# Optimization experiments

Measured on AMD Instinct MI355X. Metric: run time of the kernel, lower is better.

Reference implementation:

```python
import jax, jax.numpy as jnp
import numpy as np
from jax import lax

INPUT_DIM = 16
H1, H2 = 64, 32
OUT_DIM = 1
B, T = 4096, 168


def _uniform(key, shape, k):
    return jax.random.uniform(key, shape, jnp.float32, -k, k)


def setup_inputs() -> dict:
    key = jax.random.key(0)
    ks = jax.random.split(key, 12)
    k1 = 1.0 / np.sqrt(H1)
    k2 = 1.0 / np.sqrt(H2)
    return {
        "x": jax.random.normal(ks[0], (B, T, INPUT_DIM), jnp.float32),
        # layer 1 (PyTorch gate order: i, f, g, o)
        "W_ih1": _uniform(ks[1], (4 * H1, INPUT_DIM), k1),
        "W_hh1": _uniform(ks[2], (4 * H1, H1), k1),
        "b_ih1": _uniform(ks[3], (4 * H1,), k1),
        "b_hh1": _uniform(ks[4], (4 * H1,), k1),
        # layer 2
        "W_ih2": _uniform(ks[5], (4 * H2, H1), k2),
        "W_hh2": _uniform(ks[6], (4 * H2, H2), k2),
        "b_ih2": _uniform(ks[7], (4 * H2,), k2),
        "b_hh2": _uniform(ks[8], (4 * H2,), k2),
        # final linear
        "W_fc": _uniform(ks[9], (OUT_DIM, H2), k2),
        "b_fc": _uniform(ks[10], (OUT_DIM,), k2),
    }


def _lstm(x, W_ih, W_hh, b_ih, b_hh, hidden):
    # Precompute input-to-gate projections for all timesteps: [B, T, 4H]
    xg = jnp.einsum("btd,gd->btg", x, W_ih) + b_ih + b_hh

    def step(carry, xt):
        h, c = carry
        gates = xt + h @ W_hh.T  # [B, 4H]
        i, f, g, o = jnp.split(gates, 4, axis=-1)
        i = jax.nn.sigmoid(i)
        f = jax.nn.sigmoid(f)
        g = jnp.tanh(g)
        o = jax.nn.sigmoid(o)
        c = f * c + i * g
        h = o * jnp.tanh(c)
        return (h, c), h

    bsz = x.shape[0]
    init = (jnp.zeros((bsz, hidden), x.dtype), jnp.zeros((bsz, hidden), x.dtype))
    (_, _), hs = lax.scan(step, init, jnp.swapaxes(xg, 0, 1))  # hs: [T, B, H]
    return jnp.swapaxes(hs, 0, 1)  # [B, T, H]


def reference(x, W_ih1, W_hh1, b_ih1, b_hh1, W_ih2, W_hh2, b_ih2, b_hh2, W_fc, b_fc):
    # Dropout layers are identity at inference (p=0.2 in train only).
    h1 = _lstm(x, W_ih1, W_hh1, b_ih1, b_hh1, H1)   # [B, T, 64]
    h2 = _lstm(h1, W_ih2, W_hh2, b_ih2, b_hh2, H2)  # [B, T, 32]
    last = h2[:, -1, :]                              # [B, 32]
    return last @ W_fc.T + b_fc                      # [B, OUT_DIM]
```

## Files before the change

### kernel.cpp

```cpp
#include <hip/hip_runtime.h>


typedef __bf16 bf16x8 __attribute__((ext_vector_type(8)));
typedef float  f32x4  __attribute__((ext_vector_type(4)));

constexpr int T_SEQ = 168;
constexpr int NB    = 16;

__device__ __forceinline__ float fsig(float v)  { return __builtin_amdgcn_rcpf(1.f + __expf(-v)); }
__device__ __forceinline__ float ftanhf(float v){ return 2.f * __builtin_amdgcn_rcpf(1.f + __expf(-2.f * v)) - 1.f; }

__device__ __forceinline__ void split_bf16(float x, __bf16& hi, __bf16& lo) {
  hi = (__bf16)x;
  lo = (__bf16)(x - (float)hi);
}

__device__ __forceinline__ void load_frag8(const float* __restrict__ Wrow, int k0,
                                           bf16x8& hi, bf16x8& lo) {
#pragma unroll
  for (int j = 0; j < 8; ++j) {
    float v = Wrow[k0 + j];
    __bf16 h = (__bf16)v;
    hi[j] = h;
    lo[j] = (__bf16)(v - (float)h);
  }
}

#define MFMA(a, b, c) __builtin_amdgcn_mfma_f32_16x16x32_bf16((a), (b), (c), 0, 0, 0)

__global__ __launch_bounds__(512, 1)
void lstm_mfma_kernel(const float* __restrict__ x,
    const float* __restrict__ Wih1, const float* __restrict__ Whh1,
    const float* __restrict__ bih1, const float* __restrict__ bhh1,
    const float* __restrict__ Wih2, const float* __restrict__ Whh2,
    const float* __restrict__ bih2, const float* __restrict__ bhh2,
    const float* __restrict__ Wfc,  const float* __restrict__ bfc,
    float* __restrict__ out)
{
  __shared__ __align__(16) __bf16 sA1[2][4 * 64 * 8];
  __shared__ __align__(16) __bf16 sA2[2][2 * 64 * 8];
  __shared__ __align__(16) __bf16 sW2[8 * 4 * 64 * 8];
  __shared__ __align__(16) __bf16 sWh2[2 * 4 * 2 * 64 * 8];
  __shared__ __align__(16) float  sP[2 * 4 * 64 * 4];
  __shared__ __align__(16) float  sH2f[16 * 32];

  const int tid  = threadIdx.x;
  const int w    = tid >> 6;
  const int lane = tid & 63;
  const int q    = lane >> 4;
  const int col  = lane & 15;
  const int b0   = blockIdx.x * NB;

  const bool isL1  = (w < 4);
  const bool isL2b = (w == 4) || (w == 5);
  const bool isL2a = (w >= 6);
  const int  wl2b  = w - 4;
  const int  wl2a  = w - 6;

  bf16x8 bhh[4][4];
  bf16x8 bih[4];
  float  b1v[4] = {0.f, 0.f, 0.f, 0.f};
  if (isL1) {
#pragma unroll
    for (int g = 0; g < 4; ++g) {
      const int r = g * 64 + w * 16 + col;
      const float* Wr = Whh1 + r * 64;
      bf16x8 h0, l0, h1f, l1f;
      load_frag8(Wr, 0 * 32 + q * 8, h0, l0);
      load_frag8(Wr, 1 * 32 + q * 8, h1f, l1f);
      bhh[g][0] = h0; bhh[g][1] = h1f; bhh[g][2] = l0; bhh[g][3] = l1f;
      bf16x8 xh, xl;
      load_frag8(Wih1 + r * 16, (q & 1) * 8, xh, xl);
      bih[g] = (q < 2) ? xh : xl;
      b1v[g] = bih1[r] + bhh1[r];
    }
  }
  float b2v[4] = {0.f, 0.f, 0.f, 0.f};
  if (isL2b) {
#pragma unroll
    for (int g = 0; g < 4; ++g) {
      const int r = g * 32 + wl2b * 16 + col;
      b2v[g] = bih2[r] + bhh2[r];
    }
  }

  for (int idx = tid; idx < 8 * 4 * 64; idx += 512) {
    const int nt = idx >> 8;
    const int kb = (idx >> 6) & 3;
    const int ln = idx & 63;
    const int qq = ln >> 4, cc = ln & 15;
    const int g  = nt >> 1, wv = nt & 1;
    const int r  = g * 32 + wv * 16 + cc;
    const int k0 = (kb & 1) * 32 + qq * 8;
    bf16x8 hh, ll;
    load_frag8(Wih2 + r * 64, k0, hh, ll);
    *(bf16x8*)&sW2[((nt * 4 + kb) * 64 + ln) * 8] = (kb < 2) ? hh : ll;
  }
  for (int idx = tid; idx < 2 * 4 * 2 * 64; idx += 512) {
    const int ln = idx & 63;
    const int hl = (idx >> 6) & 1;
    const int g  = (idx >> 7) & 3;
    const int wl = idx >> 9;
    const int qq = ln >> 4, cc = ln & 15;
    const int r  = g * 32 + wl * 16 + cc;
    bf16x8 hh, ll;
    load_frag8(Whh2 + r * 32, qq * 8, hh, ll);
    *(bf16x8*)&sWh2[(((wl * 4 + g) * 2 + hl) * 64 + ln) * 8] = hl ? ll : hh;
  }

  {
    bf16x8 z;
#pragma unroll
    for (int j = 0; j < 8; ++j) z[j] = (__bf16)0.f;
    for (int i = tid; i < 2 * 4 * 64; i += 512) *(bf16x8*)&sA1[0][i * 8] = z;
    for (int i = tid; i < 2 * 2 * 64; i += 512) *(bf16x8*)&sA2[0][i * 8] = z;
  }
  __syncthreads();

  const float* xbase = x + ((size_t)(b0 + col) * T_SEQ) * 16 + (q & 1) * 8;
  float4 xcA, xcB, xnA, xnB;
  if (isL1) {
    xcA = *(const float4*)(xbase + 0);
    xcB = *(const float4*)(xbase + 4);
  }

  float c1s[4] = {0.f, 0.f, 0.f, 0.f};
  float c2s[4] = {0.f, 0.f, 0.f, 0.f};
  const int uu   = w * 16 + col;
  const int uu2b = wl2b * 16 + col;

  for (int t = 0; t <= T_SEQ; ++t) {
    const int p = t & 1;

    if (isL1 && t + 1 < T_SEQ) {
      const float* xr = xbase + (size_t)(t + 1) * 16;
      xnA = *(const float4*)(xr + 0);
      xnB = *(const float4*)(xr + 4);
    }

    if (isL2a && t >= 1) {
      const bf16x8 a2l0 = *(const bf16x8*)&sA1[p][(2 * 64 + lane) * 8];
      const bf16x8 a2l1 = *(const bf16x8*)&sA1[p][(3 * 64 + lane) * 8];
      const bf16x8 ah0  = *(const bf16x8*)&sA2[p][(0 * 64 + lane) * 8];
      const bf16x8 ah1  = *(const bf16x8*)&sA2[p][(1 * 64 + lane) * 8];
#pragma unroll
      for (int g = 0; g < 4; ++g) {
        const int nt = g * 2 + wl2a;
        const bf16x8 whi0 = *(const bf16x8*)&sW2[((nt * 4 + 0) * 64 + lane) * 8];
        const bf16x8 whi1 = *(const bf16x8*)&sW2[((nt * 4 + 1) * 64 + lane) * 8];
        const bf16x8 whh  = *(const bf16x8*)&sWh2[(((wl2a * 4 + g) * 2 + 0) * 64 + lane) * 8];
        const bf16x8 whl  = *(const bf16x8*)&sWh2[(((wl2a * 4 + g) * 2 + 1) * 64 + lane) * 8];
        f32x4 pa = {0.f, 0.f, 0.f, 0.f};
        pa = MFMA(a2l0, whi0, pa);
        pa = MFMA(a2l1, whi1, pa);
        pa = MFMA(ah0,  whh,  pa);
        pa = MFMA(ah1,  whh,  pa);
        pa = MFMA(ah0,  whl,  pa);
        *(f32x4*)&sP[((wl2a * 4 + g) * 64 + lane) * 4] = pa;
      }
    }

    f32x4 c2[4];
    if (isL2b && t >= 1) {
      const bf16x8 a2h0 = *(const bf16x8*)&sA1[p][(0 * 64 + lane) * 8];
      const bf16x8 a2h1 = *(const bf16x8*)&sA1[p][(1 * 64 + lane) * 8];
#pragma unroll
      for (int g = 0; g < 4; ++g) {
        const int nt = g * 2 + wl2b;
        const bf16x8 bb0 = *(const bf16x8*)&sW2[((nt * 4 + 0) * 64 + lane) * 8];
        const bf16x8 bb1 = *(const bf16x8*)&sW2[((nt * 4 + 1) * 64 + lane) * 8];
        const bf16x8 bb2 = *(const bf16x8*)&sW2[((nt * 4 + 2) * 64 + lane) * 8];
        const bf16x8 bb3 = *(const bf16x8*)&sW2[((nt * 4 + 3) * 64 + lane) * 8];
        c2[g][0] = b2v[g]; c2[g][1] = b2v[g]; c2[g][2] = b2v[g]; c2[g][3] = b2v[g];
        c2[g] = MFMA(a2h0, bb0, c2[g]);
        c2[g] = MFMA(a2h1, bb1, c2[g]);
        c2[g] = MFMA(a2h0, bb2, c2[g]);
        c2[g] = MFMA(a2h1, bb3, c2[g]);
      }
    }
    __syncthreads();

    if (isL1 && t < T_SEQ) {
      const float xc[8] = {xcA.x, xcA.y, xcA.z, xcA.w, xcB.x, xcB.y, xcB.z, xcB.w};
      bf16x8 xh8, xl8;
#pragma unroll
      for (int j = 0; j < 8; ++j) {
        __bf16 h, l; split_bf16(xc[j], h, l);
        xh8[j] = h; xl8[j] = l;
      }
      const bf16x8 ax0 = (q < 2) ? xh8 : xl8;
      const bf16x8 ax1 = (q < 2) ? xl8 : xh8;

      bf16x8 a1[4];
#pragma unroll
      for (int kb = 0; kb < 4; ++kb) a1[kb] = *(const bf16x8*)&sA1[p][(kb * 64 + lane) * 8];

      f32x4 c[4];
#pragma unroll
      for (int g = 0; g < 4; ++g) { c[g][0] = b1v[g]; c[g][1] = b1v[g]; c[g][2] = b1v[g]; c[g][3] = b1v[g]; }
#pragma unroll
      for (int g = 0; g < 4; ++g) {
        c[g] = MFMA(ax0,   bih[g],    c[g]);
        c[g] = MFMA(ax1,   bih[g],    c[g]);
        c[g] = MFMA(a1[0], bhh[g][0], c[g]);
        c[g] = MFMA(a1[1], bhh[g][1], c[g]);
        c[g] = MFMA(a1[2], bhh[g][0], c[g]);
        c[g] = MFMA(a1[3], bhh[g][1], c[g]);
        c[g] = MFMA(a1[0], bhh[g][2], c[g]);
        c[g] = MFMA(a1[1], bhh[g][3], c[g]);
      }
      const int kbh = uu >> 5;
      const int lnb = ((uu & 31) >> 3) * 16;
      const int jj  = uu & 7;
#pragma unroll
      for (int r = 0; r < 4; ++r) {
        const float iv = fsig(c[0][r]);
        const float fv = fsig(c[1][r]);
        const float gv = ftanhf(c[2][r]);
        const float ov = fsig(c[3][r]);
        const float cc = fmaf(fv, c1s[r], iv * gv);
        c1s[r] = cc;
        __bf16 hh, hl;
        split_bf16(ov * ftanhf(cc), hh, hl);
        const int m = q * 4 + r;
        sA1[1 - p][((kbh * 64) + lnb + m) * 8 + jj]       = hh;
        sA1[1 - p][(((2 + kbh) * 64) + lnb + m) * 8 + jj] = hl;
      }
      xcA = xnA; xcB = xnB;
    }

    if (isL2b && t >= 1) {
      const int lnb2 = ((uu2b & 31) >> 3) * 16;
      const int jj2  = uu2b & 7;
#pragma unroll
      for (int g = 0; g < 4; ++g)
        c2[g] += *(const f32x4*)&sP[((wl2b * 4 + g) * 64 + lane) * 4];
#pragma unroll
      for (int r = 0; r < 4; ++r) {
        const float iv = fsig(c2[0][r]);
        const float fv = fsig(c2[1][r]);
        const float gv = ftanhf(c2[2][r]);
        const float ov = fsig(c2[3][r]);
        const float cc = fmaf(fv, c2s[r], iv * gv);
        c2s[r] = cc;
        const float hf = ov * ftanhf(cc);
        __bf16 hh, hl;
        split_bf16(hf, hh, hl);
        const int m = q * 4 + r;
        sA2[1 - p][((0 * 64) + lnb2 + m) * 8 + jj2] = hh;
        sA2[1 - p][((1 * 64) + lnb2 + m) * 8 + jj2] = hl;
        if (t == T_SEQ) sH2f[m * 32 + uu2b] = hf;
      }
    }
    __syncthreads();
  }

  if (tid < NB) {
    float s = bfc[0];
#pragma unroll
    for (int j = 0; j < 32; ++j) s = fmaf(Wfc[j], sH2f[tid * 32 + j], s);
    out[b0 + tid] = s;
  }
}

extern "C" void kernel_launch(void* const* d_in, const int* in_sizes, int n_in,
                              void* d_out, int out_size, void* d_ws, size_t ws_size,
                              hipStream_t stream) {
  (void)in_sizes; (void)n_in; (void)out_size; (void)d_ws; (void)ws_size;
  const float* x    = (const float*)d_in[0];
  const float* Wih1 = (const float*)d_in[1];
  const float* Whh1 = (const float*)d_in[2];
  const float* bih1 = (const float*)d_in[3];
  const float* bhh1 = (const float*)d_in[4];
  const float* Wih2 = (const float*)d_in[5];
  const float* Whh2 = (const float*)d_in[6];
  const float* bih2 = (const float*)d_in[7];
  const float* bhh2 = (const float*)d_in[8];
  const float* Wfc  = (const float*)d_in[9];
  const float* bfc  = (const float*)d_in[10];
  float* out = (float*)d_out;

  hipLaunchKernelGGL(lstm_mfma_kernel, dim3(4096 / NB), dim3(512), 0, stream,
                     x, Wih1, Whh1, bih1, bhh1, Wih2, Whh2, bih2, bhh2, Wfc, bfc, out);
}
```

Measured before the change: 328.2 us.

## Pipeline layer-2 input projection one step ahead and drop one barrier per step

Restructures the per-timestep schedule. Layer-2 input-projection waves now compute W_ih2·h1 for step t into a double-buffered partial array. Layer-2 recurrent waves consume that partial one step later, together with their own W_hh2·h2 MFMAs, so layer 2 lags layer 1 by two steps. This removes the mid-iteration __syncthreads, leaving one barrier per step, and lets layer-1 and layer-2 work run concurrently. The cost is one extra loop iteration, a second sP buffer, and rebalanced MFMA counts per wave (6 on the input side, 3 on the recurrent side).

```diff
diff --git a/kernel.cpp b/kernel.cpp
--- a/kernel.cpp
+++ b/kernel.cpp
@@ -41,7 +41,7 @@
   __shared__ __align__(16) __bf16 sA2[2][2 * 64 * 8];
   __shared__ __align__(16) __bf16 sW2[8 * 4 * 64 * 8];
   __shared__ __align__(16) __bf16 sWh2[2 * 4 * 2 * 64 * 8];
-  __shared__ __align__(16) float  sP[2 * 4 * 64 * 4];
+  __shared__ __align__(16) float  sP[2][2 * 4 * 64 * 4];
   __shared__ __align__(16) float  sH2f[16 * 32];
 
   const int tid  = threadIdx.x;
@@ -129,112 +129,103 @@
   const int uu   = w * 16 + col;
   const int uu2b = wl2b * 16 + col;
 
-  for (int t = 0; t <= T_SEQ; ++t) {
+  for (int t = 0; t <= T_SEQ + 1; ++t) {
     const int p = t & 1;
 
-    if (isL1 && t + 1 < T_SEQ) {
-      const float* xr = xbase + (size_t)(t + 1) * 16;
-      xnA = *(const float4*)(xr + 0);
-      xnB = *(const float4*)(xr + 4);
-    }
-
-    if (isL2a && t >= 1) {
-      const bf16x8 a2l0 = *(const bf16x8*)&sA1[p][(2 * 64 + lane) * 8];
-      const bf16x8 a2l1 = *(const bf16x8*)&sA1[p][(3 * 64 + lane) * 8];
-      const bf16x8 ah0  = *(const bf16x8*)&sA2[p][(0 * 64 + lane) * 8];
-      const bf16x8 ah1  = *(const bf16x8*)&sA2[p][(1 * 64 + lane) * 8];
+    if (isL1) {
+      if (t + 1 < T_SEQ) {
+        const float* xr = xbase + (size_t)(t + 1) * 16;
+        xnA = *(const float4*)(xr + 0);
+        xnB = *(const float4*)(xr + 4);
+      }
+      if (t < T_SEQ) {
+        const float xc[8] = {xcA.x, xcA.y, xcA.z, xcA.w, xcB.x, xcB.y, xcB.z, xcB.w};
+        bf16x8 xh8, xl8;
+#pragma unroll
+        for (int j = 0; j < 8; ++j) {
+          __bf16 h, l; split_bf16(xc[j], h, l);
+          xh8[j] = h; xl8[j] = l;
+        }
+        const bf16x8 ax0 = (q < 2) ? xh8 : xl8;
+        const bf16x8 ax1 = (q < 2) ? xl8 : xh8;
+
+        bf16x8 a1[4];
+#pragma unroll
+        for (int kb = 0; kb < 4; ++kb) a1[kb] = *(const bf16x8*)&sA1[p][(kb * 64 + lane) * 8];
+
+        f32x4 c[4];
+#pragma unroll
+        for (int g = 0; g < 4; ++g) { c[g][0] = b1v[g]; c[g][1] = b1v[g]; c[g][2] = b1v[g]; c[g][3] = b1v[g]; }
+#pragma unroll
+        for (int g = 0; g < 4; ++g) {
+          c[g] = MFMA(ax0,   bih[g],    c[g]);
+          c[g] = MFMA(ax1,   bih[g],    c[g]);
+          c[g] = MFMA(a1[0], bhh[g][0], c[g]);
+          c[g] = MFMA(a1[1], bhh[g][1], c[g]);
+          c[g] = MFMA(a1[2], bhh[g][0], c[g]);
+          c[g] = MFMA(a1[3], bhh[g][1], c[g]);
+          c[g] = MFMA(a1[0], bhh[g][2], c[g]);
+          c[g] = MFMA(a1[1], bhh[g][3], c[g]);
+        }
+        const int kbh = uu >> 5;
+        const int lnb = ((uu & 31) >> 3) * 16;
+        const int jj  = uu & 7;
+#pragma unroll
+        for (int r = 0; r < 4; ++r) {
+          const float iv = fsig(c[0][r]);
+          const float fv = fsig(c[1][r]);
+          const float gv = ftanhf(c[2][r]);
+          const float ov = fsig(c[3][r]);
+          const float cc = fmaf(fv, c1s[r], iv * gv);
+          c1s[r] = cc;
+          __bf16 hh, hl;
+          split_bf16(ov * ftanhf(cc), hh, hl);
+          const int m = q * 4 + r;
+          sA1[1 - p][((kbh * 64) + lnb + m) * 8 + jj]       = hh;
+          sA1[1 - p][(((2 + kbh) * 64) + lnb + m) * 8 + jj] = hl;
+        }
+        xcA = xnA; xcB = xnB;
+      }
+    }
+
+    if (isL2a && t >= 1 && t <= T_SEQ) {
+      bf16x8 a2[4];
+#pragma unroll
+      for (int kb = 0; kb < 4; ++kb) a2[kb] = *(const bf16x8*)&sA1[p][(kb * 64 + lane) * 8];
 #pragma unroll
       for (int g = 0; g < 4; ++g) {
         const int nt = g * 2 + wl2a;
-        const bf16x8 whi0 = *(const bf16x8*)&sW2[((nt * 4 + 0) * 64 + lane) * 8];
-        const bf16x8 whi1 = *(const bf16x8*)&sW2[((nt * 4 + 1) * 64 + lane) * 8];
-        const bf16x8 whh  = *(const bf16x8*)&sWh2[(((wl2a * 4 + g) * 2 + 0) * 64 + lane) * 8];
-        const bf16x8 whl  = *(const bf16x8*)&sWh2[(((wl2a * 4 + g) * 2 + 1) * 64 + lane) * 8];
-        f32x4 pa = {0.f, 0.f, 0.f, 0.f};
-        pa = MFMA(a2l0, whi0, pa);
-        pa = MFMA(a2l1, whi1, pa);
-        pa = MFMA(ah0,  whh,  pa);
-        pa = MFMA(ah1,  whh,  pa);
-        pa = MFMA(ah0,  whl,  pa);
-        *(f32x4*)&sP[((wl2a * 4 + g) * 64 + lane) * 4] = pa;
-      }
-    }
-
-    f32x4 c2[4];
-    if (isL2b && t >= 1) {
-      const bf16x8 a2h0 = *(const bf16x8*)&sA1[p][(0 * 64 + lane) * 8];
-      const bf16x8 a2h1 = *(const bf16x8*)&sA1[p][(1 * 64 + lane) * 8];
-#pragma unroll
-      for (int g = 0; g < 4; ++g) {
-        const int nt = g * 2 + wl2b;
         const bf16x8 bb0 = *(const bf16x8*)&sW2[((nt * 4 + 0) * 64 + lane) * 8];
         const bf16x8 bb1 = *(const bf16x8*)&sW2[((nt * 4 + 1) * 64 + lane) * 8];
         const bf16x8 bb2 = *(const bf16x8*)&sW2[((nt * 4 + 2) * 64 + lane) * 8];
         const bf16x8 bb3 = *(const bf16x8*)&sW2[((nt * 4 + 3) * 64 + lane) * 8];
+        f32x4 pa = {0.f, 0.f, 0.f, 0.f};
+        pa = MFMA(a2[0], bb0, pa);
+        pa = MFMA(a2[1], bb1, pa);
+        pa = MFMA(a2[0], bb2, pa);
+        pa = MFMA(a2[1], bb3, pa);
+        pa = MFMA(a2[2], bb0, pa);
+        pa = MFMA(a2[3], bb1, pa);
+        *(f32x4*)&sP[p][((wl2a * 4 + g) * 64 + lane) * 4] = pa;
+      }
+    }
+
+    if (isL2b && t >= 2) {
+      const bf16x8 ah0 = *(const bf16x8*)&sA2[1 - p][(0 * 64 + lane) * 8];
+      const bf16x8 ah1 = *(const bf16x8*)&sA2[1 - p][(1 * 64 + lane) * 8];
+      f32x4 c2[4];
+#pragma unroll
+      for (int g = 0; g < 4; ++g) {
+        const bf16x8 whh = *(const bf16x8*)&sWh2[(((wl2b * 4 + g) * 2 + 0) * 64 + lane) * 8];
+        const bf16x8 whl = *(const bf16x8*)&sWh2[(((wl2b * 4 + g) * 2 + 1) * 64 + lane) * 8];
         c2[g][0] = b2v[g]; c2[g][1] = b2v[g]; c2[g][2] = b2v[g]; c2[g][3] = b2v[g];
-        c2[g] = MFMA(a2h0, bb0, c2[g]);
-        c2[g] = MFMA(a2h1, bb1, c2[g]);
-        c2[g] = MFMA(a2h0, bb2, c2[g]);
-        c2[g] = MFMA(a2h1, bb3, c2[g]);
-      }
-    }
-    __syncthreads();
-
-    if (isL1 && t < T_SEQ) {
-      const float xc[8] = {xcA.x, xcA.y, xcA.z, xcA.w, xcB.x, xcB.y, xcB.z, xcB.w};
-      bf16x8 xh8, xl8;
-#pragma unroll
-      for (int j = 0; j < 8; ++j) {
-        __bf16 h, l; split_bf16(xc[j], h, l);
-        xh8[j] = h; xl8[j] = l;
-      }
-      const bf16x8 ax0 = (q < 2) ? xh8 : xl8;
-      const bf16x8 ax1 = (q < 2) ? xl8 : xh8;
-
-      bf16x8 a1[4];
-#pragma unroll
-      for (int kb = 0; kb < 4; ++kb) a1[kb] = *(const bf16x8*)&sA1[p][(kb * 64 + lane) * 8];
-
-      f32x4 c[4];
-#pragma unroll
-      for (int g = 0; g < 4; ++g) { c[g][0] = b1v[g]; c[g][1] = b1v[g]; c[g][2] = b1v[g]; c[g][3] = b1v[g]; }
-#pragma unroll
-      for (int g = 0; g < 4; ++g) {
-        c[g] = MFMA(ax0,   bih[g],    c[g]);
-        c[g] = MFMA(ax1,   bih[g],    c[g]);
-        c[g] = MFMA(a1[0], bhh[g][0], c[g]);
-        c[g] = MFMA(a1[1], bhh[g][1], c[g]);
-        c[g] = MFMA(a1[2], bhh[g][0], c[g]);
-        c[g] = MFMA(a1[3], bhh[g][1], c[g]);
-        c[g] = MFMA(a1[0], bhh[g][2], c[g]);
-        c[g] = MFMA(a1[1], bhh[g][3], c[g]);
-      }
-      const int kbh = uu >> 5;
-      const int lnb = ((uu & 31) >> 3) * 16;
-      const int jj  = uu & 7;
-#pragma unroll
-      for (int r = 0; r < 4; ++r) {
-        const float iv = fsig(c[0][r]);
-        const float fv = fsig(c[1][r]);
-        const float gv = ftanhf(c[2][r]);
-        const float ov = fsig(c[3][r]);
-        const float cc = fmaf(fv, c1s[r], iv * gv);
-        c1s[r] = cc;
-        __bf16 hh, hl;
-        split_bf16(ov * ftanhf(cc), hh, hl);
-        const int m = q * 4 + r;
-        sA1[1 - p][((kbh * 64) + lnb + m) * 8 + jj]       = hh;
-        sA1[1 - p][(((2 + kbh) * 64) + lnb + m) * 8 + jj] = hl;
-      }
-      xcA = xnA; xcB = xnB;
-    }
-
-    if (isL2b && t >= 1) {
+        c2[g] = MFMA(ah0, whh, c2[g]);
+        c2[g] = MFMA(ah1, whh, c2[g]);
+        c2[g] = MFMA(ah0, whl, c2[g]);
+        c2[g] += *(const f32x4*)&sP[1 - p][((wl2b * 4 + g) * 64 + lane) * 4];
+      }
       const int lnb2 = ((uu2b & 31) >> 3) * 16;
       const int jj2  = uu2b & 7;
-#pragma unroll
-      for (int g = 0; g < 4; ++g)
-        c2[g] += *(const f32x4*)&sP[((wl2b * 4 + g) * 64 + lane) * 4];
 #pragma unroll
       for (int r = 0; r < 4; ++r) {
         const float iv = fsig(c2[0][r]);
@@ -247,11 +238,12 @@
         __bf16 hh, hl;
         split_bf16(hf, hh, hl);
         const int m = q * 4 + r;
-        sA2[1 - p][((0 * 64) + lnb2 + m) * 8 + jj2] = hh;
-        sA2[1 - p][((1 * 64) + lnb2 + m) * 8 + jj2] = hl;
-        if (t == T_SEQ) sH2f[m * 32 + uu2b] = hf;
-      }
-    }
+        sA2[p][((0 * 64) + lnb2 + m) * 8 + jj2] = hh;
+        sA2[p][((1 * 64) + lnb2 + m) * 8 + jj2] = hl;
+        if (t == T_SEQ + 1) sH2f[m * 32 + uu2b] = hf;
+      }
+    }
+
     __syncthreads();
   }
 
```

Result: faster. 292.7 us (-10.8%).
